# Kernel optimization log

Hardware: AMD Instinct MI355X
Metric: run time of the kernel (lower is better)

## Reference

```python
import jax, jax.numpy as jnp
import numpy as np

B, SQ, SKV, D, H = 2, 2048, 2048, 1024, 16
HD = D // H  # 64
SIGMOID_BIAS = -8.0
LN_EPS = 1e-5


def setup_inputs() -> dict:
    key = jax.random.key(0)
    ks = jax.random.split(key, 6)
    s = D ** -0.5
    return {
        "q": jax.random.normal(ks[0], (B, SQ, D), dtype=jnp.float32),
        "kv": jax.random.normal(ks[1], (B, SKV, D), dtype=jnp.float32),
        "Wq": jax.random.normal(ks[2], (D, D), dtype=jnp.float32) * s,
        "Wkv": jax.random.normal(ks[3], (D, 2 * D), dtype=jnp.float32) * s,
        "v_gamma": jnp.ones((HD,), dtype=jnp.float32),
        "v_beta": jnp.zeros((HD,), dtype=jnp.float32),
        "Wproj": jax.random.normal(ks[4], (D, D), dtype=jnp.float32) * s,
    }


def _layernorm(x, gamma, beta):
    # LayerNorm over the last dim (head_dim)
    mu = jnp.mean(x, axis=-1, keepdims=True)
    var = jnp.mean(jnp.square(x - mu), axis=-1, keepdims=True)
    return (x - mu) * jax.lax.rsqrt(var + LN_EPS) * gamma + beta


def reference(q, kv, Wq, Wkv, v_gamma, v_beta, Wproj):
    # Projections (no bias)
    qh = (q @ Wq).reshape(B, SQ, H, HD)                    # [B,Sq,H,hd]
    kvh = (kv @ Wkv).reshape(B, SKV, 2, H, HD)
    k = kvh[:, :, 0]                                       # [B,Skv,H,hd]
    v = kvh[:, :, 1]
    # v_norm is always applied (qk_norm=False -> q/k norms are identity)
    v = _layernorm(v, v_gamma, v_beta)
    # prescale: scale both q and k by head_dim ** -0.25
    scale = HD ** -0.25
    logits = jnp.einsum("bqhd,bkhd->bhqk", qh * scale, k * scale)
    # sigmoid attention (no softmax normalization), causal mask:
    # score masked where i + Skv - Sq - j < 0  <=>  j > i (equal lengths)
    iq = jnp.arange(SQ)[:, None]
    jk = jnp.arange(SKV)[None, :]
    causal_mask = (jk <= iq + (SKV - SQ)).astype(logits.dtype)  # [Sq,Skv]
    attn = jax.nn.sigmoid(logits + SIGMOID_BIAS) * causal_mask
    attn_times_v = jnp.einsum("bhqk,bkhd->bqhd", attn, v).reshape(B, SQ, D)
    attn_proj = attn_times_v @ Wproj
    return attn_times_v, attn_proj
```

## Files before the change

kernel.cpp:

```cpp
#include <hip/hip_runtime.h>
#include <hip/hip_bf16.h>

#define B_ 2
#define SQ_ 2048
#define SKV_ 2048
#define D_ 1024
#define H_ 16
#define HD_ 64

typedef unsigned short u16;
typedef float f32x4 __attribute__((ext_vector_type(4)));
typedef float f32x16 __attribute__((ext_vector_type(16)));
typedef short s16x8 __attribute__((ext_vector_type(8)));

__device__ __forceinline__ u16 f2bf(float f) {
  union { float f; unsigned u; } v; v.f = f;
  return (u16)((v.u + 0x7FFFu + ((v.u >> 16) & 1u)) >> 16);
}
__device__ __forceinline__ float bf2f(u16 h) {
  union { unsigned u; float f; } v; v.u = ((unsigned)h) << 16;
  return v.f;
}
__device__ __forceinline__ unsigned pack2bf(float s0, float s1) {
  union { float f; unsigned u; } a, b; a.f = s0; b.f = s1;
  return __builtin_amdgcn_perm(b.u + 0x8000u, a.u + 0x8000u, 0x07060302u);
}
__device__ __forceinline__ f32x4 mfma16(s16x8 a, s16x8 b, f32x4 c) {
  return __builtin_amdgcn_mfma_f32_16x16x32_bf16(a, b, c, 0, 0, 0);
}
__device__ __forceinline__ f32x16 mfma32(s16x8 a, s16x8 b, f32x16 c) {
  return __builtin_amdgcn_mfma_f32_32x32x16_bf16(a, b, c, 0, 0, 0);
}
__device__ __forceinline__ void async16(const u16* g, u16* l) {
  __builtin_amdgcn_global_load_lds(
      (const __attribute__((address_space(1))) unsigned int*)g,
      (__attribute__((address_space(3))) unsigned int*)l, 16, 0, 0);
}

__device__ __forceinline__ void tr_tile(const float* __restrict__ in, u16* __restrict__ out,
                                        int R, int C, int cx, int ry, int t) {
  __shared__ u16 tile[32][33];
  int tx = t & 31, ty = t >> 5;
  int c0 = cx * 32, r0 = ry * 32;
#pragma unroll
  for (int i = 0; i < 4; i++)
    tile[ty + i * 8][tx] = f2bf(in[(size_t)(r0 + ty + i * 8) * C + c0 + tx]);
  __syncthreads();
#pragma unroll
  for (int i = 0; i < 4; i++)
    out[(size_t)(c0 + ty + i * 8) * R + r0 + tx] = tile[tx][ty + i * 8];
}

__device__ __forceinline__ void cast4(const float* __restrict__ in, u16* __restrict__ out,
                                      int i) {
  float4 f = *(const float4*)(in + i);
  ushort4 o;
  o.x = f2bf(f.x); o.y = f2bf(f.y); o.z = f2bf(f.z); o.w = f2bf(f.w);
  *(ushort4*)(out + i) = o;
}

__global__ __launch_bounds__(256) void prep_kernel(
    const float* __restrict__ q, u16* __restrict__ q_bf,
    const float* __restrict__ kv, u16* __restrict__ kv_bf,
    const float* __restrict__ Wq, u16* __restrict__ WqT,
    const float* __restrict__ Wkv, u16* __restrict__ WkvT,
    const float* __restrict__ Wproj, u16* __restrict__ WprT) {
  int bid = blockIdx.x, t = threadIdx.x;
  if (bid < 4096) {
    cast4(q, q_bf, bid * 1024 + t * 4);
  } else if (bid < 8192) {
    cast4(kv, kv_bf, (bid - 4096) * 1024 + t * 4);
  } else if (bid < 9216) {
    int b2 = bid - 8192;
    tr_tile(Wq, WqT, 1024, 1024, b2 & 31, b2 >> 5, t);
  } else if (bid < 11264) {
    int b2 = bid - 9216;
    tr_tile(Wkv, WkvT, 1024, 2048, b2 & 63, b2 >> 6, t);
  } else {
    int b2 = bid - 11264;
    tr_tile(Wproj, WprT, 1024, 1024, b2 & 31, b2 >> 5, t);
  }
}

template <int BM, int BN, bool OUT_BF16>
__device__ __forceinline__ void gemm_body(const u16* __restrict__ A,
                                          const u16* __restrict__ BT,
                                          void* __restrict__ Cout,
                                          int m0, int n0, int N, int K) {
  __shared__ __attribute__((aligned(16))) u16 As[BM][32];
  __shared__ __attribute__((aligned(16))) u16 Bs[BN][32];
  constexpr int AM = BM / 32, AN = BN / 32;
  int t = threadIdx.x, w = t >> 6, lane = t & 63;
  int l16 = lane & 15, quad = lane >> 4;
  int mw = (w >> 1) * (BM / 2), nw = (w & 1) * (BN / 2);
  int grow = w * 16 + (lane >> 2);
  int gcol = (lane & 3) * 8;

  f32x4 acc[AM][AN] = {};

  for (int kt = 0; kt < K; kt += 32) {
    __syncthreads();
#pragma unroll
    for (int j = 0; j < BM / 64; j++)
      async16(A + (size_t)(m0 + j * 64 + grow) * K + kt + gcol, &As[j * 64 + w * 16][0]);
#pragma unroll
    for (int j = 0; j < BN / 64; j++)
      async16(BT + (size_t)(n0 + j * 64 + grow) * K + kt + gcol, &Bs[j * 64 + w * 16][0]);
    __syncthreads();
    s16x8 af[AM], bf[AN];
#pragma unroll
    for (int i = 0; i < AM; i++) af[i] = *(const s16x8*)&As[mw + i * 16 + l16][quad * 8];
#pragma unroll
    for (int j = 0; j < AN; j++) bf[j] = *(const s16x8*)&Bs[nw + j * 16 + l16][quad * 8];
#pragma unroll
    for (int i = 0; i < AM; i++)
#pragma unroll
      for (int j = 0; j < AN; j++)
        acc[i][j] = mfma16(af[i], bf[j], acc[i][j]);
  }

#pragma unroll
  for (int i = 0; i < AM; i++)
#pragma unroll
    for (int j = 0; j < AN; j++) {
      int col = n0 + nw + j * 16 + l16;
#pragma unroll
      for (int r = 0; r < 4; r++) {
        int row = m0 + mw + i * 16 + quad * 4 + r;
        float v = acc[i][j][r];
        if (OUT_BF16)
          ((u16*)Cout)[(size_t)row * N + col] = f2bf(v);
        else
          ((float*)Cout)[(size_t)row * N + col] = v;
      }
    }
}

__global__ __launch_bounds__(256, 3) void gemm_qkv(const u16* __restrict__ q_bf,
                                                   const u16* __restrict__ WqT,
                                                   u16* __restrict__ qh,
                                                   const u16* __restrict__ kv_bf,
                                                   const u16* __restrict__ WkvT,
                                                   u16* __restrict__ kvh) {
  int bx = blockIdx.x;
  if (bx < 8)
    gemm_body<128, 128, true>(q_bf, WqT, qh, blockIdx.y * 128, bx * 128, D_, D_);
  else
    gemm_body<128, 128, true>(kv_bf, WkvT, kvh, blockIdx.y * 128, (bx - 8) * 128, 2 * D_, D_);
}

__global__ __launch_bounds__(256, 3) void gemm_proj(const u16* __restrict__ A,
                                                    const u16* __restrict__ BT,
                                                    float* __restrict__ C) {
  gemm_body<64, 128, false>(A, BT, C, blockIdx.y * 64, blockIdx.x * 128, D_, D_);
}

__global__ __launch_bounds__(256) void ln_vt_kernel(const u16* __restrict__ kvh,
                                                    const float* __restrict__ gamma,
                                                    const float* __restrict__ beta,
                                                    u16* __restrict__ vt) {
  __shared__ __attribute__((aligned(16))) u16 tile[64][72];
  int bid = blockIdx.x;
  int stile = bid & 31;
  int h = (bid >> 5) & 15;
  int b = bid >> 9;
  int wave = threadIdx.x >> 6, lane = threadIdx.x & 63;
  float g = gamma[lane], be = beta[lane];
#pragma unroll 4
  for (int i = 0; i < 16; i++) {
    int s = stile * 64 + wave * 16 + i;
    float x = bf2f(kvh[(size_t)(b * SKV_ + s) * 2048 + 1024 + h * 64 + lane]);
    float sum = x;
#pragma unroll
    for (int off = 32; off; off >>= 1) sum += __shfl_xor(sum, off, 64);
    float mu = sum * (1.0f / 64.0f);
    float dx = x - mu;
    float s2 = dx * dx;
#pragma unroll
    for (int off = 32; off; off >>= 1) s2 += __shfl_xor(s2, off, 64);
    float inv = rsqrtf(s2 * (1.0f / 64.0f) + 1e-5f);
    tile[lane][wave * 16 + i] = f2bf(dx * inv * g + be);
  }
  __syncthreads();
  int d = threadIdx.x >> 2, sc = (threadIdx.x & 3) * 16;
  size_t orow = ((size_t)(b * H_ + h) * 64 + d) * SKV_ + stile * 64 + sc;
  uint4 v0 = *(const uint4*)&tile[d][sc];
  uint4 v1 = *(const uint4*)&tile[d][sc + 8];
  *(uint4*)(vt + orow) = v0;
  *(uint4*)(vt + orow + 8) = v1;
}

__global__ __launch_bounds__(256, 2) void attn_kernel(const u16* __restrict__ qh,
                                                      const u16* __restrict__ kvh,
                                                      const u16* __restrict__ vt,
                                                      float* __restrict__ out0,
                                                      u16* __restrict__ atv_bf) {
  __shared__ __attribute__((aligned(16))) u16 Ks[2][64][68];
  __shared__ __attribute__((aligned(16))) u16 Vs[2][64][68];
  __shared__ __attribute__((aligned(16))) u16 Ps[4][32][36];

  int bh = blockIdx.x;
  int qt = 31 - blockIdx.y;
  int h = bh & 15, b = bh >> 4;
  int t = threadIdx.x;
  int w = t >> 6, lane = t & 63;
  int l31 = lane & 31, hi = lane >> 5;
  int qs = w & 1, kh = w >> 1;
  int srow = t >> 2;
  int scol = (t & 3) * 16;

  const float C1 = -0.18033688011f;
  const float C2 = 11.5415603272f;

  const u16* gkb = kvh + ((size_t)(b * SKV_) + srow) * 2048 + h * 64 + scol;
  const u16* gvb = vt + ((size_t)((b * H_ + h) * 64 + srow)) * 2048 + scol;
  float* Osc = (float*)&Ks[0][0][0];

  int q0 = qt * 64;
  int nkv = qt + 1;

  s16x8 qf[4];
  {
    const u16* qp = qh + (size_t)(b * SQ_ + q0 + qs * 32 + l31) * D_ + h * 64 + hi * 8;
#pragma unroll
    for (int c = 0; c < 4; c++) qf[c] = *(const s16x8*)(qp + c * 16);
  }

  f32x16 oacc[2] = {};

  uint4 kr0 = *(const uint4*)gkb, kr1 = *(const uint4*)(gkb + 8);
  uint4 vr0 = *(const uint4*)gvb, vr1 = *(const uint4*)(gvb + 8);

  for (int kt = 0; kt < nkv; kt++) {
    int buf = kt & 1;
    *(uint4*)&Ks[buf][srow][scol] = kr0; *(uint4*)&Ks[buf][srow][scol + 8] = kr1;
    *(uint4*)&Vs[buf][srow][scol] = vr0; *(uint4*)&Vs[buf][srow][scol + 8] = vr1;
    __syncthreads();
    if (kt + 1 < nkv) {
      const u16* gk2 = gkb + (size_t)(kt + 1) * 64 * 2048;
      const u16* gv2 = gvb + (size_t)(kt + 1) * 64;
      kr0 = *(const uint4*)gk2; kr1 = *(const uint4*)(gk2 + 8);
      vr0 = *(const uint4*)gv2; vr1 = *(const uint4*)(gv2 + 8);
    }

    f32x16 st = {};
#pragma unroll
    for (int c = 0; c < 4; c++) {
      s16x8 kf = *(const s16x8*)&Ks[buf][kh * 32 + l31][c * 16 + hi * 8];
      st = mfma32(kf, qf[c], st);
    }

    if (kt == nkv - 1) {
      int qi = q0 + qs * 32 + l31;
      int kbase = kt * 64 + kh * 32 + 4 * hi;
#pragma unroll
      for (int g = 0; g < 4; g++) {
        float pv4[4];
#pragma unroll
        for (int i = 0; i < 4; i++) {
          float s = st[4 * g + i];
          float e = __builtin_amdgcn_exp2f(s * C1 + C2);
          float p = __builtin_amdgcn_rcpf(1.0f + e);
          pv4[i] = (kbase + 8 * g + i > qi) ? 0.0f : p;
        }
        uint2 pv;
        pv.x = pack2bf(pv4[0], pv4[1]);
        pv.y = pack2bf(pv4[2], pv4[3]);
        *(uint2*)&Ps[w][l31][8 * g + 4 * hi] = pv;
      }
    } else {
#pragma unroll
      for (int g = 0; g < 4; g++) {
        float pv4[4];
#pragma unroll
        for (int i = 0; i < 4; i++) {
          float s = st[4 * g + i];
          float e = __builtin_amdgcn_exp2f(s * C1 + C2);
          pv4[i] = __builtin_amdgcn_rcpf(1.0f + e);
        }
        uint2 pv;
        pv.x = pack2bf(pv4[0], pv4[1]);
        pv.y = pack2bf(pv4[2], pv4[3]);
        *(uint2*)&Ps[w][l31][8 * g + 4 * hi] = pv;
      }
    }

    s16x8 pa[2];
#pragma unroll
    for (int kc = 0; kc < 2; kc++)
      pa[kc] = *(const s16x8*)&Ps[w][l31][kc * 16 + hi * 8];
#pragma unroll
    for (int dt = 0; dt < 2; dt++)
#pragma unroll
      for (int kc = 0; kc < 2; kc++) {
        s16x8 vf = *(const s16x8*)&Vs[buf][dt * 32 + l31][kh * 32 + kc * 16 + hi * 8];
        oacc[dt] = mfma32(pa[kc], vf, oacc[dt]);
      }
  }

  __syncthreads();
  if (kh == 1) {
#pragma unroll
    for (int dt = 0; dt < 2; dt++)
#pragma unroll
      for (int reg = 0; reg < 16; reg++) {
        int ql = (reg & 3) + 8 * (reg >> 2) + 4 * hi;
        Osc[(qs * 32 + ql) * 66 + dt * 32 + l31] = oacc[dt][reg];
      }
  }
  __syncthreads();
  if (kh == 0) {
#pragma unroll
    for (int dt = 0; dt < 2; dt++)
#pragma unroll
      for (int reg = 0; reg < 16; reg++) {
        int ql = (reg & 3) + 8 * (reg >> 2) + 4 * hi;
        float v = oacc[dt][reg] + Osc[(qs * 32 + ql) * 66 + dt * 32 + l31];
        int row = q0 + qs * 32 + ql;
        int col = h * 64 + dt * 32 + l31;
        size_t idx = (size_t)(b * SQ_ + row) * D_ + col;
        out0[idx] = v;
        atv_bf[idx] = f2bf(v);
      }
  }
}

extern "C" void kernel_launch(void* const* d_in, const int* in_sizes, int n_in,
                              void* d_out, int out_size, void* d_ws, size_t ws_size,
                              hipStream_t stream) {
  const float* q      = (const float*)d_in[0];
  const float* kv     = (const float*)d_in[1];
  const float* Wq     = (const float*)d_in[2];
  const float* Wkv    = (const float*)d_in[3];
  const float* vgamma = (const float*)d_in[4];
  const float* vbeta  = (const float*)d_in[5];
  const float* Wproj  = (const float*)d_in[6];
  float* out0 = (float*)d_out;
  float* out1 = out0 + (size_t)B_ * SQ_ * D_;

  char* p = (char*)d_ws;
  u16* q_bf  = (u16*)p; p += (size_t)B_ * SQ_ * D_ * 2;
  u16* kv_bf = (u16*)p; p += (size_t)B_ * SKV_ * D_ * 2;
  u16* WqT   = (u16*)p; p += (size_t)D_ * D_ * 2;
  u16* WkvT  = (u16*)p; p += (size_t)2 * D_ * D_ * 2;
  u16* WprT  = (u16*)p; p += (size_t)D_ * D_ * 2;
  u16* qh    = (u16*)p; p += (size_t)B_ * SQ_ * D_ * 2;
  u16* kvh   = (u16*)p; p += (size_t)B_ * SKV_ * 2 * D_ * 2;
  u16* vt    = (u16*)p; p += (size_t)B_ * H_ * HD_ * SKV_ * 2;
  u16* atv   = (u16*)p; p += (size_t)B_ * SQ_ * D_ * 2;

  prep_kernel<<<dim3(12288), 256, 0, stream>>>(q, q_bf, kv, kv_bf, Wq, WqT, Wkv, WkvT, Wproj, WprT);

  gemm_qkv<<<dim3(24, 32), 256, 0, stream>>>(q_bf, WqT, qh, kv_bf, WkvT, kvh);

  ln_vt_kernel<<<dim3((B_ * H_ * SKV_) / 64), 256, 0, stream>>>(kvh, vgamma, vbeta, vt);

  attn_kernel<<<dim3(32, 32), 256, 0, stream>>>(qh, kvh, vt, out0, atv);

  gemm_proj<<<dim3(8, 64), 256, 0, stream>>>(atv, WprT, out1);
}
```

Measured before the change: 201.9 us.

## Fuse activation bf16 cast and V LayerNorm/transpose into QKV GEMM

The QKV GEMM now reads fp32 q/kv directly and converts them to bf16 while staging A tiles in shared memory, which removes the separate cast pass and its bf16 intermediate buffers. Its epilogue applies the V LayerNorm in registers using cross-lane reductions and writes V transposed straight into the vt layout. This removes the ln_vt kernel and the V half of kvh, and K goes to its own compact buffer. In exchange the GEMM loads twice as many A bytes, stages A synchronously instead of async, computes variance as E[x²]−mu² (less numerically stable), and the transposed vt stores are scattered 2-byte writes.

```diff
diff --git a/kernel.cpp b/kernel.cpp
--- a/kernel.cpp
+++ b/kernel.cpp
@@ -51,34 +51,121 @@
     out[(size_t)(c0 + ty + i * 8) * R + r0 + tx] = tile[tx][ty + i * 8];
 }
 
-__device__ __forceinline__ void cast4(const float* __restrict__ in, u16* __restrict__ out,
-                                      int i) {
-  float4 f = *(const float4*)(in + i);
-  ushort4 o;
-  o.x = f2bf(f.x); o.y = f2bf(f.y); o.z = f2bf(f.z); o.w = f2bf(f.w);
-  *(ushort4*)(out + i) = o;
-}
-
 __global__ __launch_bounds__(256) void prep_kernel(
-    const float* __restrict__ q, u16* __restrict__ q_bf,
-    const float* __restrict__ kv, u16* __restrict__ kv_bf,
     const float* __restrict__ Wq, u16* __restrict__ WqT,
     const float* __restrict__ Wkv, u16* __restrict__ WkvT,
     const float* __restrict__ Wproj, u16* __restrict__ WprT) {
   int bid = blockIdx.x, t = threadIdx.x;
-  if (bid < 4096) {
-    cast4(q, q_bf, bid * 1024 + t * 4);
-  } else if (bid < 8192) {
-    cast4(kv, kv_bf, (bid - 4096) * 1024 + t * 4);
-  } else if (bid < 9216) {
-    int b2 = bid - 8192;
-    tr_tile(Wq, WqT, 1024, 1024, b2 & 31, b2 >> 5, t);
-  } else if (bid < 11264) {
-    int b2 = bid - 9216;
+  if (bid < 1024) {
+    tr_tile(Wq, WqT, 1024, 1024, bid & 31, bid >> 5, t);
+  } else if (bid < 3072) {
+    int b2 = bid - 1024;
     tr_tile(Wkv, WkvT, 1024, 2048, b2 & 63, b2 >> 6, t);
   } else {
-    int b2 = bid - 11264;
+    int b2 = bid - 3072;
     tr_tile(Wproj, WprT, 1024, 1024, b2 & 31, b2 >> 5, t);
+  }
+}
+
+__global__ __launch_bounds__(256, 3) void gemm_qkv(
+    const float* __restrict__ q, const u16* __restrict__ WqT, u16* __restrict__ qh,
+    const float* __restrict__ kv, const u16* __restrict__ WkvT, u16* __restrict__ kb,
+    const float* __restrict__ gamma, const float* __restrict__ beta, u16* __restrict__ vt) {
+  __shared__ __attribute__((aligned(16))) u16 As[128][32];
+  __shared__ __attribute__((aligned(16))) u16 Bs[128][32];
+  int bx = blockIdx.x;
+  int m0 = blockIdx.y * 128;
+  const float* A; const u16* BT; int n0;
+  if (bx < 8) { A = q; BT = WqT; n0 = bx * 128; }
+  else        { A = kv; BT = WkvT; n0 = (bx - 8) * 128; }
+
+  int t = threadIdx.x, w = t >> 6, lane = t & 63;
+  int l16 = lane & 15, quad = lane >> 4;
+  int mw = (w >> 1) * 64, nw = (w & 1) * 64;
+  int arow = t >> 1, acol = (t & 1) * 16;
+  int grow = w * 16 + (lane >> 2);
+  int gcol = (lane & 3) * 8;
+
+  f32x4 acc[4][4] = {};
+  float4 a4[4];
+  const float* ga = A + (size_t)(m0 + arow) * 1024 + acol;
+#pragma unroll
+  for (int c = 0; c < 4; c++) a4[c] = *(const float4*)(ga + c * 4);
+
+  for (int kt = 0; kt < 1024; kt += 32) {
+    __syncthreads();
+    uint4 w0, w1;
+    w0.x = pack2bf(a4[0].x, a4[0].y); w0.y = pack2bf(a4[0].z, a4[0].w);
+    w0.z = pack2bf(a4[1].x, a4[1].y); w0.w = pack2bf(a4[1].z, a4[1].w);
+    w1.x = pack2bf(a4[2].x, a4[2].y); w1.y = pack2bf(a4[2].z, a4[2].w);
+    w1.z = pack2bf(a4[3].x, a4[3].y); w1.w = pack2bf(a4[3].z, a4[3].w);
+    *(uint4*)&As[arow][acol] = w0;
+    *(uint4*)&As[arow][acol + 8] = w1;
+#pragma unroll
+    for (int j = 0; j < 2; j++)
+      async16(BT + (size_t)(n0 + j * 64 + grow) * 1024 + kt + gcol, &Bs[j * 64 + w * 16][0]);
+    __syncthreads();
+    if (kt + 32 < 1024) {
+#pragma unroll
+      for (int c = 0; c < 4; c++) a4[c] = *(const float4*)(ga + kt + 32 + c * 4);
+    }
+    s16x8 af[4], bf[4];
+#pragma unroll
+    for (int i = 0; i < 4; i++) af[i] = *(const s16x8*)&As[mw + i * 16 + l16][quad * 8];
+#pragma unroll
+    for (int j = 0; j < 4; j++) bf[j] = *(const s16x8*)&Bs[nw + j * 16 + l16][quad * 8];
+#pragma unroll
+    for (int i = 0; i < 4; i++)
+#pragma unroll
+      for (int j = 0; j < 4; j++)
+        acc[i][j] = mfma16(af[i], bf[j], acc[i][j]);
+  }
+
+  if (bx < 16) {
+    u16* out = (bx < 8) ? qh : kb;
+#pragma unroll
+    for (int i = 0; i < 4; i++)
+#pragma unroll
+      for (int j = 0; j < 4; j++) {
+        int col = n0 + nw + j * 16 + l16;
+#pragma unroll
+        for (int r = 0; r < 4; r++) {
+          int row = m0 + mw + i * 16 + quad * 4 + r;
+          out[(size_t)row * 1024 + col] = f2bf(acc[i][j][r]);
+        }
+      }
+  } else {
+    int hh = ((n0 + nw) >> 6) - 16;
+    float gmm[4], bta[4];
+#pragma unroll
+    for (int j = 0; j < 4; j++) { gmm[j] = gamma[j * 16 + l16]; bta[j] = beta[j * 16 + l16]; }
+#pragma unroll
+    for (int i = 0; i < 4; i++)
+#pragma unroll
+      for (int r = 0; r < 4; r++) {
+        float sx = 0.0f, sxx = 0.0f;
+#pragma unroll
+        for (int j = 0; j < 4; j++) {
+          float x = acc[i][j][r];
+          sx += x; sxx += x * x;
+        }
+#pragma unroll
+        for (int off = 8; off; off >>= 1) {
+          sx += __shfl_xor(sx, off);
+          sxx += __shfl_xor(sxx, off);
+        }
+        float mu = sx * 0.015625f;
+        float var = sxx * 0.015625f - mu * mu;
+        float inv = rsqrtf(var + 1e-5f);
+        int row = m0 + mw + i * 16 + quad * 4 + r;
+        int bb = row >> 11, ss = row & 2047;
+        u16* vtp = vt + ((size_t)(bb * 16 + hh) * 64 + l16) * 2048 + ss;
+#pragma unroll
+        for (int j = 0; j < 4; j++) {
+          float y = (acc[i][j][r] - mu) * inv * gmm[j] + bta[j];
+          vtp[(size_t)(j * 16) * 2048] = f2bf(y);
+        }
+      }
   }
 }
 
@@ -136,62 +223,14 @@
     }
 }
 
-__global__ __launch_bounds__(256, 3) void gemm_qkv(const u16* __restrict__ q_bf,
-                                                   const u16* __restrict__ WqT,
-                                                   u16* __restrict__ qh,
-                                                   const u16* __restrict__ kv_bf,
-                                                   const u16* __restrict__ WkvT,
-                                                   u16* __restrict__ kvh) {
-  int bx = blockIdx.x;
-  if (bx < 8)
-    gemm_body<128, 128, true>(q_bf, WqT, qh, blockIdx.y * 128, bx * 128, D_, D_);
-  else
-    gemm_body<128, 128, true>(kv_bf, WkvT, kvh, blockIdx.y * 128, (bx - 8) * 128, 2 * D_, D_);
-}
-
 __global__ __launch_bounds__(256, 3) void gemm_proj(const u16* __restrict__ A,
                                                     const u16* __restrict__ BT,
                                                     float* __restrict__ C) {
   gemm_body<64, 128, false>(A, BT, C, blockIdx.y * 64, blockIdx.x * 128, D_, D_);
 }
 
-__global__ __launch_bounds__(256) void ln_vt_kernel(const u16* __restrict__ kvh,
-                                                    const float* __restrict__ gamma,
-                                                    const float* __restrict__ beta,
-                                                    u16* __restrict__ vt) {
-  __shared__ __attribute__((aligned(16))) u16 tile[64][72];
-  int bid = blockIdx.x;
-  int stile = bid & 31;
-  int h = (bid >> 5) & 15;
-  int b = bid >> 9;
-  int wave = threadIdx.x >> 6, lane = threadIdx.x & 63;
-  float g = gamma[lane], be = beta[lane];
-#pragma unroll 4
-  for (int i = 0; i < 16; i++) {
-    int s = stile * 64 + wave * 16 + i;
-    float x = bf2f(kvh[(size_t)(b * SKV_ + s) * 2048 + 1024 + h * 64 + lane]);
-    float sum = x;
-#pragma unroll
-    for (int off = 32; off; off >>= 1) sum += __shfl_xor(sum, off, 64);
-    float mu = sum * (1.0f / 64.0f);
-    float dx = x - mu;
-    float s2 = dx * dx;
-#pragma unroll
-    for (int off = 32; off; off >>= 1) s2 += __shfl_xor(s2, off, 64);
-    float inv = rsqrtf(s2 * (1.0f / 64.0f) + 1e-5f);
-    tile[lane][wave * 16 + i] = f2bf(dx * inv * g + be);
-  }
-  __syncthreads();
-  int d = threadIdx.x >> 2, sc = (threadIdx.x & 3) * 16;
-  size_t orow = ((size_t)(b * H_ + h) * 64 + d) * SKV_ + stile * 64 + sc;
-  uint4 v0 = *(const uint4*)&tile[d][sc];
-  uint4 v1 = *(const uint4*)&tile[d][sc + 8];
-  *(uint4*)(vt + orow) = v0;
-  *(uint4*)(vt + orow + 8) = v1;
-}
-
 __global__ __launch_bounds__(256, 2) void attn_kernel(const u16* __restrict__ qh,
-                                                      const u16* __restrict__ kvh,
+                                                      const u16* __restrict__ kb,
                                                       const u16* __restrict__ vt,
                                                       float* __restrict__ out0,
                                                       u16* __restrict__ atv_bf) {
@@ -212,7 +251,7 @@
   const float C1 = -0.18033688011f;
   const float C2 = 11.5415603272f;
 
-  const u16* gkb = kvh + ((size_t)(b * SKV_) + srow) * 2048 + h * 64 + scol;
+  const u16* gkb = kb + ((size_t)(b * SKV_) + srow) * 1024 + h * 64 + scol;
   const u16* gvb = vt + ((size_t)((b * H_ + h) * 64 + srow)) * 2048 + scol;
   float* Osc = (float*)&Ks[0][0][0];
 
@@ -237,7 +276,7 @@
     *(uint4*)&Vs[buf][srow][scol] = vr0; *(uint4*)&Vs[buf][srow][scol + 8] = vr1;
     __syncthreads();
     if (kt + 1 < nkv) {
-      const u16* gk2 = gkb + (size_t)(kt + 1) * 64 * 2048;
+      const u16* gk2 = gkb + (size_t)(kt + 1) * 64 * 1024;
       const u16* gv2 = gvb + (size_t)(kt + 1) * 64;
       kr0 = *(const uint4*)gk2; kr1 = *(const uint4*)(gk2 + 8);
       vr0 = *(const uint4*)gv2; vr1 = *(const uint4*)(gv2 + 8);
@@ -339,23 +378,19 @@
   float* out1 = out0 + (size_t)B_ * SQ_ * D_;
 
   char* p = (char*)d_ws;
-  u16* q_bf  = (u16*)p; p += (size_t)B_ * SQ_ * D_ * 2;
-  u16* kv_bf = (u16*)p; p += (size_t)B_ * SKV_ * D_ * 2;
-  u16* WqT   = (u16*)p; p += (size_t)D_ * D_ * 2;
-  u16* WkvT  = (u16*)p; p += (size_t)2 * D_ * D_ * 2;
-  u16* WprT  = (u16*)p; p += (size_t)D_ * D_ * 2;
-  u16* qh    = (u16*)p; p += (size_t)B_ * SQ_ * D_ * 2;
-  u16* kvh   = (u16*)p; p += (size_t)B_ * SKV_ * 2 * D_ * 2;
-  u16* vt    = (u16*)p; p += (size_t)B_ * H_ * HD_ * SKV_ * 2;
-  u16* atv   = (u16*)p; p += (size_t)B_ * SQ_ * D_ * 2;
-
-  prep_kernel<<<dim3(12288), 256, 0, stream>>>(q, q_bf, kv, kv_bf, Wq, WqT, Wkv, WkvT, Wproj, WprT);
-
-  gemm_qkv<<<dim3(24, 32), 256, 0, stream>>>(q_bf, WqT, qh, kv_bf, WkvT, kvh);
-
-  ln_vt_kernel<<<dim3((B_ * H_ * SKV_) / 64), 256, 0, stream>>>(kvh, vgamma, vbeta, vt);
-
-  attn_kernel<<<dim3(32, 32), 256, 0, stream>>>(qh, kvh, vt, out0, atv);
+  u16* WqT  = (u16*)p; p += (size_t)D_ * D_ * 2;
+  u16* WkvT = (u16*)p; p += (size_t)2 * D_ * D_ * 2;
+  u16* WprT = (u16*)p; p += (size_t)D_ * D_ * 2;
+  u16* qh   = (u16*)p; p += (size_t)B_ * SQ_ * D_ * 2;
+  u16* kb   = (u16*)p; p += (size_t)B_ * SKV_ * D_ * 2;
+  u16* vt   = (u16*)p; p += (size_t)B_ * H_ * HD_ * SKV_ * 2;
+  u16* atv  = (u16*)p; p += (size_t)B_ * SQ_ * D_ * 2;
+
+  prep_kernel<<<dim3(4096), 256, 0, stream>>>(Wq, WqT, Wkv, WkvT, Wproj, WprT);
+
+  gemm_qkv<<<dim3(24, 32), 256, 0, stream>>>(q, WqT, qh, kv, WkvT, kb, vgamma, vbeta, vt);
+
+  attn_kernel<<<dim3(32, 32), 256, 0, stream>>>(qh, kb, vt, out0, atv);
 
   gemm_proj<<<dim3(8, 64), 256, 0, stream>>>(atv, WprT, out1);
 }
```

After: 202.2 us. About the same (+0.2%).
